# Kernel tuning notes

Hardware: AMD Instinct MI355X
Metric: run time of the kernel (lower is better)

The kernel has to match this reference:

```python
import jax, jax.numpy as jnp
import numpy as np

B, N, E, H = 2, 2048, 1024, 16
HD = E // H  # head_dim = 64


def setup_inputs() -> dict:
    key = jax.random.key(0)
    k1, k2, k3, k4, k5 = jax.random.split(key, 5)
    x = jax.random.normal(k1, (B, N, E), dtype=jnp.float32)
    # per-head Linear(E, 3*HD): stacked weights [H, E, 3*HD] and biases [H, 3*HD]
    Wqkv = jax.random.normal(k2, (H, E, 3 * HD), dtype=jnp.float32) * (1.0 / np.sqrt(E))
    bqkv = jax.random.normal(k3, (H, 3 * HD), dtype=jnp.float32) * 0.01
    Wout = jax.random.normal(k4, (E, E), dtype=jnp.float32) * (1.0 / np.sqrt(E))
    bout = jax.random.normal(k5, (E,), dtype=jnp.float32) * 0.01
    return {"x": x, "Wqkv": Wqkv, "bqkv": bqkv, "Wout": Wout, "bout": bout}


def reference(x, Wqkv, bqkv, Wout, bout):
    # per-head QKV projection, vectorized over heads: [B, H, N, 3*HD]
    proj = jnp.einsum('bne,hef->bhnf', x, Wqkv) + bqkv[None, :, None, :]
    k, q, v = jnp.split(proj, 3, axis=-1)  # each [B, H, N, HD]
    # scores = q @ k^T / sqrt(HD): [B, H, N, N]
    scores = jnp.einsum('bhqd,bhkd->bhqk', q, k) / jnp.sqrt(jnp.asarray(HD, dtype=x.dtype))
    # causal mask (tril)
    causal = jnp.tril(jnp.ones((N, N), dtype=bool))
    scores = jnp.where(causal[None, None, :, :], scores, -jnp.inf)
    attn = jax.nn.softmax(scores, axis=-1)
    sa = jnp.einsum('bhqk,bhkd->bhqd', attn, v)  # [B, H, N, HD]
    # concat heads in order -> [B, N, E]
    sa = jnp.transpose(sa, (0, 2, 1, 3)).reshape(B, N, E)
    return sa @ Wout + bout
```

## Files before the change

kernel.cpp:

```cpp
#include <hip/hip_runtime.h>
#include <hip/hip_bf16.h>

#define Bz 2
#define Nn 2048
#define Ee 1024
#define Hh 16
#define HD 64

typedef unsigned short u16;
typedef unsigned int u32;

typedef __bf16 bf16x8 __attribute__((ext_vector_type(8)));
typedef float f32x4 __attribute__((ext_vector_type(4)));

__device__ __forceinline__ float bf2f(u16 u) {
    u32 v = ((u32)u) << 16;
    return __builtin_bit_cast(float, v);
}
__device__ __forceinline__ u16 f2bf(float f) {
    u32 i = __builtin_bit_cast(u32, f);
    u32 r = (i + 0x7FFFu + ((i >> 16) & 1u)) >> 16;
    return (u16)r;
}
__device__ __forceinline__ u32 pack2(float a, float b) {
    return (u32)f2bf(a) | ((u32)f2bf(b) << 16);
}
__device__ __forceinline__ bf16x8 ld_frag(const u16* p) {
    return __builtin_bit_cast(bf16x8, *(const uint4*)p);
}
__device__ __forceinline__ f32x4 zero4() {
    f32x4 z; z[0]=0.f; z[1]=0.f; z[2]=0.f; z[3]=0.f; return z;
}

__device__ __forceinline__ void async_copy16(const u16* g, u16* l) {
    __builtin_amdgcn_global_load_lds(
        (const __attribute__((address_space(1))) u32*)g,
        (__attribute__((address_space(3))) u32*)l, 16, 0, 0);
}

__global__ void ws_diag(float* out, float code) { out[0] = code; }

__global__ __launch_bounds__(256) void convert_x(
    const float* __restrict__ x, u16* __restrict__ xbf)
{
    size_t idx = ((size_t)blockIdx.x * 256 + threadIdx.x) * 8;
    float4 f0 = *(const float4*)(x + idx);
    float4 f1 = *(const float4*)(x + idx + 4);
    uint4 pk;
    pk.x = pack2(f0.x, f0.y); pk.y = pack2(f0.z, f0.w);
    pk.z = pack2(f1.x, f1.y); pk.w = pack2(f1.z, f1.w);
    *(uint4*)(xbf + idx) = pk;
}

__global__ __launch_bounds__(256) void transpose_f32_bf16(
    const float* __restrict__ src, u16* __restrict__ dst, int R, int C)
{
    const int r0 = blockIdx.x * 64, c0 = blockIdx.y * 64;
    const size_t zoff = (size_t)blockIdx.z * R * C;
    src += zoff; dst += zoff;
    const int tid = threadIdx.x;

    __shared__ float T[64][65];
    {
        int tr = tid >> 2, tc = (tid & 3) * 16;
        const float* s = src + (size_t)(r0 + tr) * C + c0 + tc;
#pragma unroll
        for (int j = 0; j < 4; ++j) {
            float4 v = ((const float4*)s)[j];
            T[tr][tc + 4 * j + 0] = v.x; T[tr][tc + 4 * j + 1] = v.y;
            T[tr][tc + 4 * j + 2] = v.z; T[tr][tc + 4 * j + 3] = v.w;
        }
    }
    __syncthreads();
    {
        int cc = tid >> 2, rr = (tid & 3) * 16;
        u16* d = dst + (size_t)(c0 + cc) * R + r0 + rr;
        u32 w[8];
#pragma unroll
        for (int i = 0; i < 8; ++i)
            w[i] = pack2(T[rr + 2 * i][cc], T[rr + 2 * i + 1][cc]);
        *(uint4*)(d)     = make_uint4(w[0], w[1], w[2], w[3]);
        *(uint4*)(d + 8) = make_uint4(w[4], w[5], w[6], w[7]);
    }
}

__global__ __launch_bounds__(256) void qkv_mfma(
    const u16* __restrict__ xbf, const u16* __restrict__ Wt,
    const float* __restrict__ bias,
    u16* __restrict__ kbuf, u16* __restrict__ qbuf, u16* __restrict__ vbuf)
{
    const int mt = blockIdx.x;
    const int h  = blockIdx.y;
    const int tid = threadIdx.x;
    const int lane = tid & 63, wid = tid >> 6;
    const int quad = lane >> 4, l15 = lane & 15;

    __shared__ u16 As[64 * 64];
    __shared__ u16 Bs[192 * 64];

    f32x4 acc[4][3];
#pragma unroll
    for (int mi = 0; mi < 4; ++mi)
#pragma unroll
        for (int ni = 0; ni < 3; ++ni) acc[mi][ni] = zero4();

    const u16* xb = xbf + (size_t)mt * 64 * Ee;
    const u16* wtb = Wt + (size_t)h * 192 * 1024;

    const int arowl = lane >> 3;
    const int jj = (lane & 7) ^ arowl;

    for (int kb = 0; kb < 16; ++kb) {
        __syncthreads();
#pragma unroll
        for (int i = 0; i < 2; ++i) {
            int rbase = (wid * 2 + i) * 8;
            const u16* g = xb + (size_t)(rbase + arowl) * Ee + kb * 64 + jj * 8;
            async_copy16(g, &As[(wid * 2 + i) * 512]);
        }
#pragma unroll
        for (int i = 0; i < 6; ++i) {
            int rbase = (wid * 6 + i) * 8;
            const u16* g = wtb + (size_t)(rbase + arowl) * 1024 + kb * 64 + jj * 8;
            async_copy16(g, &Bs[(wid * 6 + i) * 512]);
        }
        __syncthreads();

#pragma unroll
        for (int kk0 = 0; kk0 < 2; ++kk0) {
            const int pos = ((kk0 * 4 + quad) ^ (l15 & 7)) * 8;
            bf16x8 af[4], bf[3];
#pragma unroll
            for (int mi = 0; mi < 4; ++mi)
                af[mi] = ld_frag(&As[(mi * 16 + l15) * 64 + pos]);
#pragma unroll
            for (int ni = 0; ni < 3; ++ni)
                bf[ni] = ld_frag(&Bs[(wid * 48 + ni * 16 + l15) * 64 + pos]);
#pragma unroll
            for (int mi = 0; mi < 4; ++mi)
#pragma unroll
                for (int ni = 0; ni < 3; ++ni)
                    acc[mi][ni] = __builtin_amdgcn_mfma_f32_16x16x32_bf16(
                        af[mi], bf[ni], acc[mi][ni], 0, 0, 0);
        }
    }

#pragma unroll
    for (int ni = 0; ni < 3; ++ni) {
        int col = wid * 48 + ni * 16 + l15;
        int ft = col >> 6, d = col & 63;
        u16* dst = (ft == 0) ? kbuf : (ft == 1) ? qbuf : vbuf;
        float bv = bias[h * 192 + col];
#pragma unroll
        for (int mi = 0; mi < 4; ++mi)
#pragma unroll
            for (int r = 0; r < 4; ++r) {
                int gm = mt * 64 + mi * 16 + quad * 4 + r;
                int bb = gm >> 11, n = gm & (Nn - 1);
                dst[(((size_t)(bb * Hh + h)) * Nn + n) * HD + d] =
                    f2bf(acc[mi][ni][r] + bv);
            }
    }
}

__global__ __launch_bounds__(256) void attn2(
    const u16* __restrict__ qbuf, const u16* __restrict__ kbuf,
    const u16* __restrict__ vbuf, u16* __restrict__ sabuf)
{
    const int p  = blockIdx.x;
    const int bh = blockIdx.y;
    const int b = bh >> 4, h = bh & 15;
    const int tid = threadIdx.x;
    const int lane = tid & 63, wid = tid >> 6;
    const int l15 = lane & 15, quad = lane >> 4;

    __shared__ u16 Ks[64][72];
    __shared__ u16 Vt[64][72];

    const u16* qb = qbuf + (size_t)bh * Nn * HD;
    const u16* kb = kbuf + (size_t)bh * Nn * HD;
    const u16* vb = vbuf + (size_t)bh * Nn * HD;

    const int skey = tid >> 2, sdq = (tid & 3) * 16;
    const int vkey = tid & 63, vd = (tid >> 6) * 16;

    const int src0 = l15 + (quad & 1) * 32;
    const bool qhi = quad >= 2;

    for (int hx = 0; hx < 2; ++hx) {
        const int qt = hx ? (31 - p) : p;
        const int nkt = qt + 1;
        const int qrow = qt * 64 + wid * 16 + l15;

        bf16x8 qf[2];
#pragma unroll
        for (int st = 0; st < 2; ++st)
            qf[st] = __builtin_bit_cast(bf16x8,
                *(const uint4*)(qb + (size_t)qrow * HD + st * 32 + quad * 8));

        f32x4 oacc[4];
#pragma unroll
        for (int dt = 0; dt < 4; ++dt) oacc[dt] = zero4();
        float m_i = -3e38f, l_i = 0.f;

        for (int kt = 0; kt < nkt; ++kt) {
            __syncthreads();
            {
                const u16* ksrc = kb + (size_t)(kt * 64 + skey) * HD + sdq;
                *(uint4*)&Ks[skey][sdq]     = *(const uint4*)(ksrc);
                *(uint4*)&Ks[skey][sdq + 8] = *(const uint4*)(ksrc + 8);
                const u16* vsrc = vb + (size_t)(kt * 64 + vkey) * HD + vd;
                uint4 a = *(const uint4*)(vsrc);
                uint4 c = *(const uint4*)(vsrc + 8);
                u32 w[8] = {a.x, a.y, a.z, a.w, c.x, c.y, c.z, c.w};
#pragma unroll
                for (int j = 0; j < 8; ++j) {
                    Vt[vd + 2 * j][vkey]     = (u16)(w[j] & 0xFFFFu);
                    Vt[vd + 2 * j + 1][vkey] = (u16)(w[j] >> 16);
                }
            }
            __syncthreads();

            f32x4 s[4];
#pragma unroll
            for (int t = 0; t < 4; ++t) {
                f32x4 a = zero4();
#pragma unroll
                for (int st = 0; st < 2; ++st) {
                    bf16x8 kf = ld_frag(&Ks[t * 16 + l15][st * 32 + quad * 8]);
                    a = __builtin_amdgcn_mfma_f32_16x16x32_bf16(kf, qf[st], a, 0, 0, 0);
                }
                s[t] = a;
            }

            const bool dn = (kt == qt);
#pragma unroll
            for (int t = 0; t < 4; ++t)
#pragma unroll
                for (int r = 0; r < 4; ++r) {
                    int key = kt * 64 + t * 16 + quad * 4 + r;
                    float v = s[t][r] * 0.125f;
                    if (dn && key > qrow) v = -3e38f;
                    s[t][r] = v;
                }

            float mx = s[0][0];
#pragma unroll
            for (int t = 0; t < 4; ++t)
#pragma unroll
                for (int r = 0; r < 4; ++r) mx = fmaxf(mx, s[t][r]);
            mx = fmaxf(mx, __shfl_xor(mx, 16));
            mx = fmaxf(mx, __shfl_xor(mx, 32));
            float mn = fmaxf(m_i, mx);
            float alpha = __expf(m_i - mn);
            m_i = mn;
            float rs = 0.f;
#pragma unroll
            for (int t = 0; t < 4; ++t)
#pragma unroll
                for (int r = 0; r < 4; ++r) {
                    float e = __expf(s[t][r] - mn);
                    s[t][r] = e;
                    rs += e;
                }
            rs += __shfl_xor(rs, 16);
            rs += __shfl_xor(rs, 32);
            l_i = l_i * alpha + rs;
#pragma unroll
            for (int dt = 0; dt < 4; ++dt)
#pragma unroll
                for (int r = 0; r < 4; ++r) oacc[dt][r] *= alpha;

            u32 pk[4][2];
#pragma unroll
            for (int t = 0; t < 4; ++t) {
                pk[t][0] = pack2(s[t][0], s[t][1]);
                pk[t][1] = pack2(s[t][2], s[t][3]);
            }
#pragma unroll
            for (int st = 0; st < 2; ++st) {
                u32 e0 = pk[2 * st][0],     e1 = pk[2 * st][1];
                u32 o0 = pk[2 * st + 1][0], o1 = pk[2 * st + 1][1];
                u32 A0 = __shfl(e0, src0),      B0 = __shfl(o0, src0);
                u32 A1 = __shfl(e1, src0),      B1 = __shfl(o1, src0);
                u32 A2 = __shfl(e0, src0 + 16), B2 = __shfl(o0, src0 + 16);
                u32 A3 = __shfl(e1, src0 + 16), B3 = __shfl(o1, src0 + 16);
                u32 U0 = qhi ? B0 : A0;
                u32 U1 = qhi ? B1 : A1;
                u32 U2 = qhi ? B2 : A2;
                u32 U3 = qhi ? B3 : A3;
                bf16x8 pf = __builtin_bit_cast(bf16x8, make_uint4(U0, U1, U2, U3));
#pragma unroll
                for (int dt = 0; dt < 4; ++dt) {
                    bf16x8 vf = ld_frag(&Vt[dt * 16 + l15][st * 32 + quad * 8]);
                    oacc[dt] = __builtin_amdgcn_mfma_f32_16x16x32_bf16(
                        vf, pf, oacc[dt], 0, 0, 0);
                }
            }
        }

        float inv = 1.f / l_i;
#pragma unroll
        for (int dt = 0; dt < 4; ++dt) {
            ushort4 ov;
            ov.x = f2bf(oacc[dt][0] * inv);
            ov.y = f2bf(oacc[dt][1] * inv);
            ov.z = f2bf(oacc[dt][2] * inv);
            ov.w = f2bf(oacc[dt][3] * inv);
            *(ushort4*)&sabuf[((size_t)(b * Nn + qrow)) * Ee + h * 64 +
                              dt * 16 + quad * 4] = ov;
        }
    }
}

typedef float f32x16 __attribute__((ext_vector_type(16)));
__device__ __forceinline__ f32x16 zero16() {
    f32x16 z;
#pragma unroll
    for (int i = 0; i < 16; ++i) z[i] = 0.f;
    return z;
}

__global__ __launch_bounds__(256) void out_mfma(
    const u16* __restrict__ A, const u16* __restrict__ Wt,
    const float* __restrict__ bias, float* __restrict__ out)
{
    const int mt = blockIdx.x;
    const int nt = blockIdx.y;
    const int tid = threadIdx.x;
    const int lane = tid & 63, wid = tid >> 6;
    const int l31 = lane & 31, khalf = (lane >> 5) * 8;

    __shared__ u16 As[128][72];
    __shared__ u16 Bs[64][72];

    f32x16 acc[2];
    acc[0] = zero16(); acc[1] = zero16();

    const u16* ab = A + (size_t)mt * 128 * Ee;
    const int arow = tid >> 1, akh = (tid & 1) * 32;
    const int brow = tid >> 2, bc = (tid & 3) * 16;

    for (int k0 = 0; k0 < Ee; k0 += 64) {
        __syncthreads();
        {
            const u16* asrc = ab + (size_t)arow * Ee + k0 + akh;
#pragma unroll
            for (int j = 0; j < 4; ++j)
                *(uint4*)&As[arow][akh + 8 * j] = *(const uint4*)(asrc + 8 * j);
            const u16* bsrc = Wt + (size_t)(nt * 64 + brow) * 1024 + k0 + bc;
            *(uint4*)&Bs[brow][bc]     = *(const uint4*)(bsrc);
            *(uint4*)&Bs[brow][bc + 8] = *(const uint4*)(bsrc + 8);
        }
        __syncthreads();
#pragma unroll
        for (int kc = 0; kc < 4; ++kc) {
            bf16x8 af = ld_frag(&As[wid * 32 + l31][kc * 16 + khalf]);
#pragma unroll
            for (int ct = 0; ct < 2; ++ct) {
                bf16x8 bf = ld_frag(&Bs[ct * 32 + l31][kc * 16 + khalf]);
                acc[ct] = __builtin_amdgcn_mfma_f32_32x32x16_bf16(af, bf, acc[ct], 0, 0, 0);
            }
        }
    }

#pragma unroll
    for (int ct = 0; ct < 2; ++ct) {
        int col = nt * 64 + ct * 32 + l31;
        float bv = bias[col];
#pragma unroll
        for (int r = 0; r < 16; ++r) {
            int row_l = (r & 3) + 8 * (r >> 2) + 4 * (lane >> 5);
            int gm = mt * 128 + wid * 32 + row_l;
            out[(size_t)gm * Ee + col] = acc[ct][r] + bv;
        }
    }
}

extern "C" void kernel_launch(void* const* d_in, const int* in_sizes, int n_in,
                              void* d_out, int out_size, void* d_ws, size_t ws_size,
                              hipStream_t stream) {
    const float* x    = (const float*)d_in[0];
    const float* Wqkv = (const float*)d_in[1];
    const float* bqkv = (const float*)d_in[2];
    const float* Wout = (const float*)d_in[3];
    const float* bout = (const float*)d_in[4];
    float* out = (float*)d_out;

    const size_t SZ = (size_t)Bz * Hh * Nn * HD;
    const size_t NSA = (size_t)Bz * Nn * Ee;
    const size_t NEED = (3 * SZ + NSA) * sizeof(u16);

    if (ws_size < NEED) {
        ws_diag<<<1, 1, 0, stream>>>(out, 20000.0f + (float)(ws_size >> 20));
        return;
    }

    u16* ws = (u16*)d_ws;
    u16* kbuf  = ws;
    u16* qbuf  = ws + SZ;
    u16* vbuf  = ws + 2 * SZ;
    u16* sabuf = ws + 3 * SZ;
    u16* wqkv_t = sabuf;
    u16* wout_t = kbuf;
    u16* xbf    = (u16*)d_out;

    convert_x<<<2048, 256, 0, stream>>>(x, xbf);
    transpose_f32_bf16<<<dim3(16, 3, 16), 256, 0, stream>>>(Wqkv, wqkv_t, 1024, 192);
    qkv_mfma<<<dim3(64, 16), 256, 0, stream>>>(xbf, wqkv_t, bqkv, kbuf, qbuf, vbuf);
    attn2<<<dim3(16, 32), 256, 0, stream>>>(qbuf, kbuf, vbuf, sabuf);
    transpose_f32_bf16<<<dim3(16, 16, 1), 256, 0, stream>>>(Wout, wout_t, 1024, 1024);
    out_mfma<<<dim3(32, 16), 256, 0, stream>>>(sabuf, wout_t, bout, out);
}
```

Measured before the change: 208.8 us.

## Double-buffer K/V tiles with async copies and pre-transposed V in attention

Adds a separate kernel that transposes V into a [HD, N] layout ahead of time. The attention kernel can then stream both K and V tiles with 16-byte async global-to-LDS copies into double-buffered, XOR-swizzled shared memory, prefetching the next tile while the current one is computed. This removes the per-element scalar LDS transpose stores and the second barrier per tile. The softmax scale is folded into a log2 constant so it can use exp2f. The cost is an extra transpose kernel launch plus one read and one write of V, and a larger LDS footprint per block.

Result: no change. 210.5 us (+0.8%).

```diff
diff --git a/kernel.cpp b/kernel.cpp
--- a/kernel.cpp
+++ b/kernel.cpp
@@ -84,6 +84,35 @@
     }
 }
 
+__global__ __launch_bounds__(256) void transpose_v(
+    const u16* __restrict__ src, u16* __restrict__ dst)
+{
+    const int n0 = blockIdx.x * 64;
+    const size_t z = blockIdx.y;
+    src += z * (size_t)Nn * HD;
+    dst += z * (size_t)HD * Nn;
+    const int tid = threadIdx.x;
+
+    __shared__ u16 T[64][66];
+    {
+        int tr = tid >> 2, tc = (tid & 3) * 16;
+        const u16* s = src + (size_t)(n0 + tr) * HD + tc;
+        *(uint4*)&T[tr][tc]     = *(const uint4*)(s);
+        *(uint4*)&T[tr][tc + 8] = *(const uint4*)(s + 8);
+    }
+    __syncthreads();
+    {
+        int cc = tid >> 2, rr = (tid & 3) * 16;
+        u32 w[8];
+#pragma unroll
+        for (int i = 0; i < 8; ++i)
+            w[i] = (u32)T[rr + 2 * i][cc] | ((u32)T[rr + 2 * i + 1][cc] << 16);
+        u16* d = dst + (size_t)cc * Nn + n0 + rr;
+        *(uint4*)(d)     = make_uint4(w[0], w[1], w[2], w[3]);
+        *(uint4*)(d + 8) = make_uint4(w[4], w[5], w[6], w[7]);
+    }
+}
+
 __global__ __launch_bounds__(256) void qkv_mfma(
     const u16* __restrict__ xbf, const u16* __restrict__ Wt,
     const float* __restrict__ bias,
@@ -165,7 +194,7 @@
 
 __global__ __launch_bounds__(256) void attn2(
     const u16* __restrict__ qbuf, const u16* __restrict__ kbuf,
-    const u16* __restrict__ vbuf, u16* __restrict__ sabuf)
+    const u16* __restrict__ vtb, u16* __restrict__ sabuf)
 {
     const int p  = blockIdx.x;
     const int bh = blockIdx.y;
@@ -174,18 +203,21 @@
     const int lane = tid & 63, wid = tid >> 6;
     const int l15 = lane & 15, quad = lane >> 4;
 
-    __shared__ u16 Ks[64][72];
-    __shared__ u16 Vt[64][72];
+    __shared__ u16 KsL[2][4096];
+    __shared__ u16 VtL[2][4096];
 
     const u16* qb = qbuf + (size_t)bh * Nn * HD;
     const u16* kb = kbuf + (size_t)bh * Nn * HD;
-    const u16* vb = vbuf + (size_t)bh * Nn * HD;
-
-    const int skey = tid >> 2, sdq = (tid & 3) * 16;
-    const int vkey = tid & 63, vd = (tid >> 6) * 16;
+    const u16* vt = vtb + (size_t)bh * HD * Nn;
+
+    const int r_l = lane >> 3;
+    const int jj = (lane & 7) ^ r_l;
+    const int xsw = l15 & 7;
 
     const int src0 = l15 + (quad & 1) * 32;
     const bool qhi = quad >= 2;
+
+    const float SC = 0.18033688f;
 
     for (int hx = 0; hx < 2; ++hx) {
         const int qt = hx ? (31 - p) : p;
@@ -203,23 +235,39 @@
         for (int dt = 0; dt < 4; ++dt) oacc[dt] = zero4();
         float m_i = -3e38f, l_i = 0.f;
 
+        __syncthreads();
+#pragma unroll
+        for (int i = 0; i < 4; ++i) {
+            int idx = wid * 4 + i;
+            if (idx < 8) {
+                const u16* g = kb + (size_t)(idx * 8 + r_l) * HD + jj * 8;
+                async_copy16(g, &KsL[0][idx * 512]);
+            } else {
+                int ii = idx - 8;
+                const u16* g = vt + (size_t)(ii * 8 + r_l) * Nn + jj * 8;
+                async_copy16(g, &VtL[0][ii * 512]);
+            }
+        }
+
         for (int kt = 0; kt < nkt; ++kt) {
             __syncthreads();
-            {
-                const u16* ksrc = kb + (size_t)(kt * 64 + skey) * HD + sdq;
-                *(uint4*)&Ks[skey][sdq]     = *(const uint4*)(ksrc);
-                *(uint4*)&Ks[skey][sdq + 8] = *(const uint4*)(ksrc + 8);
-                const u16* vsrc = vb + (size_t)(kt * 64 + vkey) * HD + vd;
-                uint4 a = *(const uint4*)(vsrc);
-                uint4 c = *(const uint4*)(vsrc + 8);
-                u32 w[8] = {a.x, a.y, a.z, a.w, c.x, c.y, c.z, c.w};
-#pragma unroll
-                for (int j = 0; j < 8; ++j) {
-                    Vt[vd + 2 * j][vkey]     = (u16)(w[j] & 0xFFFFu);
-                    Vt[vd + 2 * j + 1][vkey] = (u16)(w[j] >> 16);
+            if (kt + 1 < nkt) {
+                const int nb = (kt + 1) & 1;
+#pragma unroll
+                for (int i = 0; i < 4; ++i) {
+                    int idx = wid * 4 + i;
+                    if (idx < 8) {
+                        const u16* g = kb + (size_t)((kt + 1) * 64 + idx * 8 + r_l) * HD + jj * 8;
+                        async_copy16(g, &KsL[nb][idx * 512]);
+                    } else {
+                        int ii = idx - 8;
+                        const u16* g = vt + (size_t)(ii * 8 + r_l) * Nn + (kt + 1) * 64 + jj * 8;
+                        async_copy16(g, &VtL[nb][ii * 512]);
+                    }
                 }
             }
-            __syncthreads();
+            const u16* K = KsL[kt & 1];
+            const u16* V = VtL[kt & 1];
 
             f32x4 s[4];
 #pragma unroll
@@ -227,7 +275,8 @@
                 f32x4 a = zero4();
 #pragma unroll
                 for (int st = 0; st < 2; ++st) {
-                    bf16x8 kf = ld_frag(&Ks[t * 16 + l15][st * 32 + quad * 8]);
+                    bf16x8 kf = ld_frag(&K[(t * 16 + l15) * 64 +
+                                           ((st * 4 + quad) ^ xsw) * 8]);
                     a = __builtin_amdgcn_mfma_f32_16x16x32_bf16(kf, qf[st], a, 0, 0, 0);
                 }
                 s[t] = a;
@@ -239,7 +288,7 @@
 #pragma unroll
                 for (int r = 0; r < 4; ++r) {
                     int key = kt * 64 + t * 16 + quad * 4 + r;
-                    float v = s[t][r] * 0.125f;
+                    float v = s[t][r] * SC;
                     if (dn && key > qrow) v = -3e38f;
                     s[t][r] = v;
                 }
@@ -252,14 +301,14 @@
             mx = fmaxf(mx, __shfl_xor(mx, 16));
             mx = fmaxf(mx, __shfl_xor(mx, 32));
             float mn = fmaxf(m_i, mx);
-            float alpha = __expf(m_i - mn);
+            float alpha = exp2f(m_i - mn);
             m_i = mn;
             float rs = 0.f;
 #pragma unroll
             for (int t = 0; t < 4; ++t)
 #pragma unroll
                 for (int r = 0; r < 4; ++r) {
-                    float e = __expf(s[t][r] - mn);
+                    float e = exp2f(s[t][r] - mn);
                     s[t][r] = e;
                     rs += e;
                 }
@@ -292,7 +341,8 @@
                 bf16x8 pf = __builtin_bit_cast(bf16x8, make_uint4(U0, U1, U2, U3));
 #pragma unroll
                 for (int dt = 0; dt < 4; ++dt) {
-                    bf16x8 vf = ld_frag(&Vt[dt * 16 + l15][st * 32 + quad * 8]);
+                    bf16x8 vf = ld_frag(&V[(dt * 16 + l15) * 64 +
+                                           ((st * 4 + quad) ^ xsw) * 8]);
                     oacc[dt] = __builtin_amdgcn_mfma_f32_16x16x32_bf16(
                         vf, pf, oacc[dt], 0, 0, 0);
                 }
@@ -404,11 +454,13 @@
     u16* wqkv_t = sabuf;
     u16* wout_t = kbuf;
     u16* xbf    = (u16*)d_out;
+    u16* vtb    = (u16*)d_out + SZ;
 
     convert_x<<<2048, 256, 0, stream>>>(x, xbf);
     transpose_f32_bf16<<<dim3(16, 3, 16), 256, 0, stream>>>(Wqkv, wqkv_t, 1024, 192);
     qkv_mfma<<<dim3(64, 16), 256, 0, stream>>>(xbf, wqkv_t, bqkv, kbuf, qbuf, vbuf);
-    attn2<<<dim3(16, 32), 256, 0, stream>>>(qbuf, kbuf, vbuf, sabuf);
+    transpose_v<<<dim3(32, 32), 256, 0, stream>>>(vbuf, vtb);
+    attn2<<<dim3(16, 32), 256, 0, stream>>>(qbuf, kbuf, vtb, sabuf);
     transpose_f32_bf16<<<dim3(16, 16, 1), 256, 0, stream>>>(Wout, wout_t, 1024, 1024);
     out_mfma<<<dim3(32, 16), 256, 0, stream>>>(sabuf, wout_t, bout, out);
 }
```
